# Performance work log

Measured on AMD Instinct MI355X. Metric: run time of the kernel, lower is better.

Reference implementation:

```python
import jax, jax.numpy as jnp
import numpy as np

N = 50000   # nodes
E = 800000  # edges (before self loops)
G = 8       # graphs in batch
IN, H, HD = 3, 64, 128


def setup_inputs() -> dict:
    key = jax.random.key(0)
    ks = jax.random.split(key, 12)
    s = 0.1  # weight scale
    return {
        "x": jax.random.normal(ks[0], (N, IN), jnp.float32),
        "edge_index": jax.random.randint(ks[1], (2, E), 0, N, dtype=jnp.int32),
        "batch": jnp.sort(jax.random.randint(ks[2], (N,), 0, G, dtype=jnp.int32)),
        "W1": s * jax.random.normal(ks[3], (IN, H), jnp.float32),
        "a_src1": s * jax.random.normal(ks[4], (H,), jnp.float32),
        "a_dst1": s * jax.random.normal(ks[5], (H,), jnp.float32),
        "b1": jnp.zeros((H,), jnp.float32),
        "W2": s * jax.random.normal(ks[6], (H, H), jnp.float32),
        "a_src2": s * jax.random.normal(ks[7], (H,), jnp.float32),
        "a_dst2": s * jax.random.normal(ks[8], (H,), jnp.float32),
        "b2": jnp.zeros((H,), jnp.float32),
        "Wh1": s * jax.random.normal(ks[9], (H, HD), jnp.float32),
        "bh1": jnp.zeros((HD,), jnp.float32),
        "Wh2": s * jax.random.normal(ks[10], (HD, 1), jnp.float32),
        "bh2": jnp.zeros((1,), jnp.float32),
    }


def gat_conv(x, src, dst, W, a_src, a_dst, b, n_nodes):
    """Single-head GATConv (PyG defaults: slope 0.2, self-loops, bias)."""
    h = x @ W                           # [N, H]
    e_s = h @ a_src                     # [N] per-node source logits
    e_d = h @ a_dst                     # [N] per-node target logits
    e = jax.nn.leaky_relu(e_s[src] + e_d[dst], 0.2)  # [E']
    # segment softmax over incoming edges of each target node
    m = jax.ops.segment_max(e, dst, num_segments=n_nodes)
    ex = jnp.exp(e - m[dst])
    denom = jax.ops.segment_sum(ex, dst, num_segments=n_nodes)
    alpha = ex / denom[dst]             # [E']
    out = jax.ops.segment_sum(h[src] * alpha[:, None], dst, num_segments=n_nodes)
    return out + b


def reference(x, edge_index, batch, W1, a_src1, a_dst1, b1,
              W2, a_src2, a_dst2, b2, Wh1, bh1, Wh2, bh2):
    n = x.shape[0]
    loops = jnp.arange(n, dtype=edge_index.dtype)
    src = jnp.concatenate([edge_index[0], loops])  # add self loops
    dst = jnp.concatenate([edge_index[1], loops])

    h = jax.nn.relu(gat_conv(x, src, dst, W1, a_src1, a_dst1, b1, n))
    h = jax.nn.relu(gat_conv(h, src, dst, W2, a_src2, a_dst2, b2, n))

    # global mean pool per graph
    sums = jax.ops.segment_sum(h, batch, num_segments=G)          # [G, H]
    cnt = jax.ops.segment_sum(jnp.ones((n,), h.dtype), batch, num_segments=G)
    pooled = sums / jnp.maximum(cnt, 1.0)[:, None]

    # value head: Linear -> ReLU -> Linear
    return jax.nn.relu(pooled @ Wh1 + bh1) @ Wh2 + bh2            # [G, 1]
```

## Files before the change

kernel.cpp:

```cpp
#include <hip/hip_runtime.h>
#include <math.h>

#define NN 50000
#define NE 800000
#define NG 8
#define H 64
#define HD 128
#define CAP 48
#define NSLICE 64
#define EPT 8
#define ETH (NE / EPT)
#define ECHUNKS ((ETH + 255) / 256)
#define NODEB ((NN * H) / 256)
#define NPB 1536
#define GB 2500
#define GSTRIDE (GB * 4)
#define NBUCK 200
#define BNODES 250
#define RCAP 4800
#define LCAP 32
#define ZWORDS (NBUCK + NSLICE*NG*H + NSLICE*NG)

typedef unsigned short ushort_t;
typedef _Float16 half_t;
typedef _Float16 half2_t __attribute__((ext_vector_type(2)));
typedef int int4v __attribute__((ext_vector_type(4)));

__global__ void k_zero(unsigned* __restrict__ p) {
    int i = blockIdx.x * blockDim.x + threadIdx.x;
    for (; i < ZWORDS; i += gridDim.x * blockDim.x) p[i] = 0u;
}

__global__ void k_binA(const int* __restrict__ src, const int* __restrict__ dst,
                       unsigned* __restrict__ cursor, unsigned* __restrict__ recs) {
    __shared__ unsigned lcnt[NBUCK];
    __shared__ unsigned lbuf[NBUCK][LCAP];
    int bid = blockIdx.x;
    for (int i = threadIdx.x; i < NBUCK; i += 256) lcnt[i] = 0;
    __syncthreads();
    int t = bid * 256 + threadIdx.x;
    int e0 = t * EPT;
    if (e0 < NE) {
        int4v da = *(const int4v*)(dst + e0);
        int4v db = *(const int4v*)(dst + e0 + 4);
        int4v sa = *(const int4v*)(src + e0);
        int4v sb = *(const int4v*)(src + e0 + 4);
        int ds[8] = {da.x, da.y, da.z, da.w, db.x, db.y, db.z, db.w};
        int ss[8] = {sa.x, sa.y, sa.z, sa.w, sb.x, sb.y, sb.z, sb.w};
        #pragma unroll
        for (int i = 0; i < 8; ++i) {
            unsigned d = (unsigned)ds[i];
            unsigned bk = d / BNODES;
            unsigned dloc = d - bk * BNODES;
            unsigned rec = ((unsigned)ss[i] << 8) | dloc;
            unsigned l = atomicAdd(&lcnt[bk], 1u);
            if (l < LCAP) lbuf[bk][l] = rec;
            else {
                unsigned g = atomicAdd(&cursor[bk], 1u);
                if (g < RCAP) recs[(size_t)bk * RCAP + g] = rec;
            }
        }
    }
    __syncthreads();
    for (int b = threadIdx.x; b < NBUCK; b += 256) {
        unsigned c = lcnt[b]; c = c > LCAP ? LCAP : c;
        if (c) {
            unsigned base = atomicAdd(&cursor[b], c);
            for (unsigned i = 0; i < c; ++i)
                if (base + i < RCAP) recs[(size_t)b * RCAP + base + i] = lbuf[b][i];
        }
    }
}

__global__ void k_buildB(const unsigned* __restrict__ cursor, const unsigned* __restrict__ recs,
                         ushort_t* __restrict__ csr, int* __restrict__ deg,
                         const float* __restrict__ x, const float* __restrict__ W,
                         const float* __restrict__ asrc, const float* __restrict__ adst,
                         const float* __restrict__ W2, half2_t* __restrict__ W2p,
                         half_t* __restrict__ h, float* __restrict__ es, float* __restrict__ ed) {
    __shared__ unsigned lcnt[BNODES];
    __shared__ ushort_t lcsr[BNODES * CAP];
    int bid = blockIdx.x;
    if (bid < NBUCK) {
        int b = bid;
        for (int i = threadIdx.x; i < BNODES; i += 256) lcnt[i] = 0;
        __syncthreads();
        unsigned total = cursor[b]; if (total > RCAP) total = RCAP;
        for (unsigned i = threadIdx.x; i < total; i += 256) {
            unsigned rec = recs[(size_t)b * RCAP + i];
            unsigned dloc = rec & 255u;
            unsigned srcv = rec >> 8;
            unsigned slot = atomicAdd(&lcnt[dloc], 1u);
            if (slot < CAP) lcsr[dloc * CAP + slot] = (ushort_t)srcv;
        }
        __syncthreads();
        const unsigned* ls = (const unsigned*)lcsr;
        unsigned* gc = (unsigned*)(csr + (size_t)b * BNODES * CAP);
        for (int i = threadIdx.x; i < BNODES * CAP / 2; i += 256) gc[i] = ls[i];
        for (int d = threadIdx.x; d < BNODES; d += 256) {
            unsigned c = lcnt[d];
            deg[b * BNODES + d] = c > CAP ? CAP : (int)c;
        }
    } else if (bid < NBUCK + NPB) {
        for (int nb = bid - NBUCK; nb < NODEB; nb += NPB) {
            int nid = nb * 256 + threadIdx.x;
            int node = nid >> 6, lane = nid & 63;
            if (node < NN) {
                float x0 = x[node*3+0], x1 = x[node*3+1], x2 = x[node*3+2];
                float hv = x0*W[lane] + x1*W[64+lane] + x2*W[128+lane];
                __builtin_nontemporal_store((half_t)hv, h + (size_t)node*64 + lane);
                float s = hv * asrc[lane], d = hv * adst[lane];
                #pragma unroll
                for (int o = 32; o > 0; o >>= 1) { s += __shfl_xor(s, o); d += __shfl_xor(d, o); }
                if (lane == 0) { es[node] = s; ed[node] = d; }
            }
        }
    } else {
        for (int i = threadIdx.x; i < (H/2) * 64; i += 256) {
            int k2 = i >> 6, ln = i & 63;
            half2_t v;
            v.x = (_Float16)W2[(2*k2)*64 + ln];
            v.y = (_Float16)W2[(2*k2+1)*64 + ln];
            W2p[i] = v;
        }
    }
}

#define GPREFETCH(node_nx)                                                       \
    int nN = 0, s0N = 0; float hsN = 0.f, ednN = 0.f, esnN = 0.f, esgN = 0.f;    \
    if ((node_nx) < NN) {                                                        \
        nN   = deg[node_nx];                                                     \
        hsN  = (float)hH[(size_t)(node_nx)*64 + lane];                           \
        ednN = ed[node_nx]; esnN = es[node_nx];                                  \
        s0N  = csr[(size_t)(node_nx) * CAP + lane];                              \
        esgN = es[s0N];                                                          \
    }

#define GPROLOGUE(node0)                                                         \
    int nC = 0, s0C = 0; float hsC = 0.f, ednC = 0.f, esnC = 0.f, esgC = 0.f;    \
    if ((node0) < NN) {                                                          \
        nC   = deg[node0]; nC = nC > CAP ? CAP : nC;                             \
        hsC  = (float)hH[(size_t)(node0)*64 + lane];                             \
        ednC = ed[node0]; esnC = es[node0];                                      \
        s0C  = csr[(size_t)(node0) * CAP + lane];                                \
        esgC = es[s0C];                                                          \
    }

#define GROTATE                                                                  \
    nC = nN > CAP ? CAP : nN; s0C = s0N; hsC = hsN; ednC = ednN; esnC = esnN;    \
    esgC = esgN;

#define CHUNK1(c)                                                                \
    {                                                                            \
        int r = (c) * 4 + sub;                                                   \
        float q = (r < nC) ? sp[r] : 0.f;                                        \
        int idx = (r < nC) ? sidx[r] : 0;                                        \
        float2 raw = *(const float2*)(hH + (size_t)idx * 64 + c4);               \
        union { float2 f; half_t hh[4]; } u; u.f = raw;                          \
        acc[(c) & 3].x += (float)u.hh[0] * q;                                    \
        acc[(c) & 3].y += (float)u.hh[1] * q;                                    \
        acc[(c) & 3].z += (float)u.hh[2] * q;                                    \
        acc[(c) & 3].w += (float)u.hh[3] * q;                                    \
        dq += q;                                                                 \
    }

#define GATHER_BODY                                                              \
    float e0 = esgC + ednC;                                                      \
    e0 = e0 > 0.f ? e0 : 0.2f * e0;                                              \
    float p0 = (lane < nC) ? __expf(e0) : 0.f;                                   \
    float evs = esnC + ednC; evs = evs > 0.f ? evs : 0.2f * evs;                 \
    float ps = __expf(evs);                                                      \
    sidx[lane] = s0C; sp[lane] = p0;                                             \
    int sub = lane >> 4;                                                         \
    int c4  = (lane & 15) * 4;                                                   \
    float4 acc[4];                                                               \
    acc[0] = {0,0,0,0}; acc[1] = {0,0,0,0}; acc[2] = {0,0,0,0}; acc[3] = {0,0,0,0}; \
    float dq = 0.f;                                                              \
    CHUNK1(0) CHUNK1(1) CHUNK1(2) CHUNK1(3)                                      \
    if (nC > 16) { CHUNK1(4) CHUNK1(5) CHUNK1(6) CHUNK1(7) }                     \
    if (nC > 32) { CHUNK1(8) CHUNK1(9) CHUNK1(10) CHUNK1(11) }                   \
    float4 A;                                                                    \
    A.x = acc[0].x + acc[1].x + acc[2].x + acc[3].x;                             \
    A.y = acc[0].y + acc[1].y + acc[2].y + acc[3].y;                             \
    A.z = acc[0].z + acc[1].z + acc[2].z + acc[3].z;                             \
    A.w = acc[0].w + acc[1].w + acc[2].w + acc[3].w;                             \
    _Pragma("unroll")                                                            \
    for (int o = 16; o <= 32; o <<= 1) {                                         \
        A.x += __shfl_xor(A.x, o); A.y += __shfl_xor(A.y, o);                    \
        A.z += __shfl_xor(A.z, o); A.w += __shfl_xor(A.w, o);                    \
        dq  += __shfl_xor(dq, o);                                                \
    }                                                                            \
    float inv = 1.0f / (dq + ps);                                                \
    float chs;                                                                   \
    {                                                                            \
        int srcl = lane >> 2;                                                    \
        float v0 = __shfl(A.x, srcl);                                            \
        float v1 = __shfl(A.y, srcl);                                            \
        float v2 = __shfl(A.z, srcl);                                            \
        float v3 = __shfl(A.w, srcl);                                            \
        int j = lane & 3;                                                        \
        chs = (j == 0) ? v0 : (j == 1) ? v1 : (j == 2) ? v2 : v3;                \
    }                                                                            \
    float f = fmaxf((chs + ps * hsC) * inv + bl, 0.f);

__global__ void k_gather1(const int* __restrict__ deg, const ushort_t* __restrict__ csr,
                          const float* __restrict__ es, const float* __restrict__ ed,
                          const half_t* __restrict__ hH, const float* __restrict__ b,
                          const half2_t* __restrict__ W2p, const float* __restrict__ as2,
                          const float* __restrict__ ad2,
                          half_t* __restrict__ h2, float* __restrict__ es2,
                          float* __restrict__ ed2) {
    __shared__ int     s_idx[4][64];
    __shared__ float   s_p[4][64];
    __shared__ half2_t s_fh[4][32];
    int lane = threadIdx.x & 63, w = threadIdx.x >> 6;
    int*   sidx = s_idx[w];
    float* sp   = s_p[w];
    float bl = b[lane], as2l = as2[lane], ad2l = ad2[lane];

    int node0 = blockIdx.x * 4 + w;
    GPROLOGUE(node0)
    for (int node = node0; node < NN; node += GSTRIDE) {
        GPREFETCH(node + GSTRIDE)
        GATHER_BODY

        ((half_t*)s_fh[w])[lane] = (half_t)f;
        float hv = 0.f;
        #pragma unroll
        for (int k2 = 0; k2 < 32; ++k2) {
            half2_t w2v = W2p[k2*64 + lane];
            half2_t f2  = s_fh[w][k2];
#if __has_builtin(__builtin_amdgcn_fdot2)
            hv = __builtin_amdgcn_fdot2(f2, w2v, hv, false);
#else
            hv += (float)f2.x * (float)w2v.x + (float)f2.y * (float)w2v.y;
#endif
        }
        h2[(size_t)node*64 + lane] = (half_t)hv;
        float ss = hv * as2l, dd = hv * ad2l;
        #pragma unroll
        for (int o = 32; o > 0; o >>= 1) {
            ss += __shfl_xor(ss, o); dd += __shfl_xor(dd, o);
        }
        if (lane == 0) { es2[node] = ss; ed2[node] = dd; }
        GROTATE
    }
}

__global__ void k_gather2(const int* __restrict__ deg, const ushort_t* __restrict__ csr,
                          const float* __restrict__ es, const float* __restrict__ ed,
                          const half_t* __restrict__ hH, const float* __restrict__ b,
                          const int* __restrict__ batch,
                          float* __restrict__ sums, float* __restrict__ cnt) {
    __shared__ int   s_idx[4][64];
    __shared__ float s_p[4][64];
    __shared__ float part[NG * H];
    __shared__ float pc[NG];
    for (int i = threadIdx.x; i < NG * H; i += 256) part[i] = 0.f;
    if (threadIdx.x < NG) pc[threadIdx.x] = 0.f;
    __syncthreads();

    int lane = threadIdx.x & 63, w = threadIdx.x >> 6;
    int*   sidx = s_idx[w];
    float* sp   = s_p[w];
    float bl = b[lane];

    int node0 = blockIdx.x * 4 + w;
    GPROLOGUE(node0)
    int gC = (node0 < NN) ? batch[node0] : 0;
    for (int node = node0; node < NN; node += GSTRIDE) {
        GPREFETCH(node + GSTRIDE)
        int gN = (node + GSTRIDE < NN) ? batch[node + GSTRIDE] : 0;
        GATHER_BODY

        atomicAdd(&part[gC * H + lane], f);
        if (lane == 0) atomicAdd(&pc[gC], 1.f);
        GROTATE
        gC = gN;
    }
    __syncthreads();
    int slice = blockIdx.x & (NSLICE - 1);
    float* ssum = sums + (size_t)slice * (NG * H);
    float* scnt = cnt + (size_t)slice * NG;
    for (int i = threadIdx.x; i < NG * H; i += 256) atomicAdd(&ssum[i], part[i]);
    if (threadIdx.x < NG) atomicAdd(&scnt[threadIdx.x], pc[threadIdx.x]);
}

__global__ void k_head(const float* __restrict__ sums, const float* __restrict__ cnt,
                       const float* __restrict__ Wh1, const float* __restrict__ bh1,
                       const float* __restrict__ Wh2, const float* __restrict__ bh2,
                       float* __restrict__ out) {
    __shared__ float pooled[NG * H];
    __shared__ float hidden[NG * HD];
    __shared__ float c_s[NG];
    int t = threadIdx.x;
    if (t < NG) {
        float c = 0.f;
        for (int s = 0; s < NSLICE; ++s) c += cnt[s * NG + t];
        c_s[t] = fmaxf(c, 1.f);
    }
    __syncthreads();
    for (int i = t; i < NG * H; i += blockDim.x) {
        float v = 0.f;
        for (int s = 0; s < NSLICE; ++s) v += sums[(size_t)s * (NG * H) + i];
        pooled[i] = v / c_s[i >> 6];
    }
    __syncthreads();
    for (int i = t; i < NG * HD; i += blockDim.x) {
        int g = i / HD, hd = i % HD;
        float acc = bh1[hd];
        for (int c = 0; c < H; ++c) acc += pooled[g * H + c] * Wh1[c * HD + hd];
        hidden[i] = fmaxf(acc, 0.f);
    }
    __syncthreads();
    if (t < NG) {
        float acc = bh2[0];
        for (int hd = 0; hd < HD; ++hd) acc += hidden[t * HD + hd] * Wh2[hd];
        out[t] = acc;
    }
}

extern "C" void kernel_launch(void* const* d_in, const int* in_sizes, int n_in,
                              void* d_out, int out_size, void* d_ws, size_t ws_size,
                              hipStream_t stream) {
    const float* x    = (const float*)d_in[0];
    const int*   ei   = (const int*)d_in[1];
    const int*   batch= (const int*)d_in[2];
    const float* W1   = (const float*)d_in[3];
    const float* as1  = (const float*)d_in[4];
    const float* ad1  = (const float*)d_in[5];
    const float* b1   = (const float*)d_in[6];
    const float* W2   = (const float*)d_in[7];
    const float* as2  = (const float*)d_in[8];
    const float* ad2  = (const float*)d_in[9];
    const float* b2   = (const float*)d_in[10];
    const float* Wh1  = (const float*)d_in[11];
    const float* bh1  = (const float*)d_in[12];
    const float* Wh2  = (const float*)d_in[13];
    const float* bh2  = (const float*)d_in[14];
    const int* src = ei;
    const int* dst = ei + NE;

    float* ws   = (float*)d_ws;
    half_t* h1  = (half_t*)ws;
    half_t* h2  = (half_t*)(ws + (size_t)NN*32);
    float* es1  = ws + (size_t)NN*64;
    float* ed1  = es1 + NN;
    float* es2  = ed1 + NN;
    float* ed2  = es2 + NN;
    unsigned* cursor = (unsigned*)(ed2 + NN);
    float* sums = (float*)(cursor + NBUCK);
    float* cnt  = sums + (size_t)NSLICE*NG*H;
    int*   deg  = (int*)(cnt + NSLICE*NG);
    ushort_t* csr = (ushort_t*)(deg + NN);
    half2_t* W2p  = (half2_t*)(csr + (size_t)NN*CAP);
    unsigned* recs = (unsigned*)(W2p + (H/2)*64);

    dim3 blk(256);
    int bBlocks = NBUCK + NPB + 1;

    k_zero<<<64, blk, 0, stream>>>(cursor);
    k_binA<<<ECHUNKS, blk, 0, stream>>>(src, dst, cursor, recs);
    k_buildB<<<bBlocks, blk, 0, stream>>>(cursor, recs, csr, deg,
                                          x, W1, as1, ad1, W2, W2p, h1, es1, ed1);
    k_gather1<<<GB, blk, 0, stream>>>(deg, csr, es1, ed1, h1, b1, W2p, as2, ad2,
                                      h2, es2, ed2);
    k_gather2<<<GB, blk, 0, stream>>>(deg, csr, es2, ed2, h2, b2, batch, sums, cnt);
    k_head<<<1, 256, 0, stream>>>(sums, cnt, Wh1, bh1, Wh2, bh2, (float*)d_out);
}
```

Baseline: 124.1 us.

## Prefetch first 16 neighbor feature rows for next node via double-buffered index smem

Extends the software pipeline in both gather kernels so the first four chunks of neighbor feature rows for the next node are loaded during the current node's work. Neighbor indices go into a second shared buffer that swaps each iteration. The aim is to hide the latency of the dependent csr→hH gather. The cost is more registers and shared memory, and the prologue no longer bounds-checks node0, which is safe only because the grid size guarantees node0 < NN.

Result: faster. 120.3 us (-3.1%).

```diff
diff --git a/kernel.cpp b/kernel.cpp
--- a/kernel.cpp
+++ b/kernel.cpp
@@ -126,29 +126,51 @@
     }
 }
 
+
+#define GPROLOGUE(node0)                                                         \
+    int nC = deg[node0]; nC = nC > CAP ? CAP : nC;                               \
+    float hsC = (float)hH[(size_t)(node0)*64 + lane];                            \
+    float ednC = ed[node0], esnC = es[node0];                                    \
+    int s0C = csr[(size_t)(node0) * CAP + lane];                                 \
+    float esgC = es[s0C];                                                        \
+    sidx[lane] = s0C;                                                            \
+    float2 t0C = *(const float2*)(hH + (size_t)sidx[sub]      * 64 + c4);        \
+    float2 t1C = *(const float2*)(hH + (size_t)sidx[4 + sub]  * 64 + c4);        \
+    float2 t2C = *(const float2*)(hH + (size_t)sidx[8 + sub]  * 64 + c4);        \
+    float2 t3C = *(const float2*)(hH + (size_t)sidx[12 + sub] * 64 + c4);
+
 #define GPREFETCH(node_nx)                                                       \
     int nN = 0, s0N = 0; float hsN = 0.f, ednN = 0.f, esnN = 0.f, esgN = 0.f;    \
+    float2 t0N = {0,0}, t1N = {0,0}, t2N = {0,0}, t3N = {0,0};                   \
     if ((node_nx) < NN) {                                                        \
         nN   = deg[node_nx];                                                     \
         hsN  = (float)hH[(size_t)(node_nx)*64 + lane];                           \
         ednN = ed[node_nx]; esnN = es[node_nx];                                  \
         s0N  = csr[(size_t)(node_nx) * CAP + lane];                              \
         esgN = es[s0N];                                                          \
-    }
-
-#define GPROLOGUE(node0)                                                         \
-    int nC = 0, s0C = 0; float hsC = 0.f, ednC = 0.f, esnC = 0.f, esgC = 0.f;    \
-    if ((node0) < NN) {                                                          \
-        nC   = deg[node0]; nC = nC > CAP ? CAP : nC;                             \
-        hsC  = (float)hH[(size_t)(node0)*64 + lane];                             \
-        ednC = ed[node0]; esnC = es[node0];                                      \
-        s0C  = csr[(size_t)(node0) * CAP + lane];                                \
-        esgC = es[s0C];                                                          \
+        sidxN[lane] = s0N;                                                       \
+        t0N = *(const float2*)(hH + (size_t)sidxN[sub]      * 64 + c4);          \
+        t1N = *(const float2*)(hH + (size_t)sidxN[4 + sub]  * 64 + c4);          \
+        t2N = *(const float2*)(hH + (size_t)sidxN[8 + sub]  * 64 + c4);          \
+        t3N = *(const float2*)(hH + (size_t)sidxN[12 + sub] * 64 + c4);          \
     }
 
 #define GROTATE                                                                  \
     nC = nN > CAP ? CAP : nN; s0C = s0N; hsC = hsN; ednC = ednN; esnC = esnN;    \
-    esgC = esgN;
+    esgC = esgN; t0C = t0N; t1C = t1N; t2C = t2N; t3C = t3N;                     \
+    { int* tmp_ = sidx; sidx = sidxN; sidxN = tmp_; }
+
+#define CHUNKP(c, tv)                                                            \
+    {                                                                            \
+        int r = (c) * 4 + sub;                                                   \
+        float q = (r < nC) ? sp[r] : 0.f;                                        \
+        union { float2 f; half_t hh[4]; } u; u.f = (tv);                         \
+        acc[(c) & 3].x += (float)u.hh[0] * q;                                    \
+        acc[(c) & 3].y += (float)u.hh[1] * q;                                    \
+        acc[(c) & 3].z += (float)u.hh[2] * q;                                    \
+        acc[(c) & 3].w += (float)u.hh[3] * q;                                    \
+        dq += q;                                                                 \
+    }
 
 #define CHUNK1(c)                                                                \
     {                                                                            \
@@ -170,13 +192,11 @@
     float p0 = (lane < nC) ? __expf(e0) : 0.f;                                   \
     float evs = esnC + ednC; evs = evs > 0.f ? evs : 0.2f * evs;                 \
     float ps = __expf(evs);                                                      \
-    sidx[lane] = s0C; sp[lane] = p0;                                             \
-    int sub = lane >> 4;                                                         \
-    int c4  = (lane & 15) * 4;                                                   \
+    sp[lane] = p0;                                                               \
     float4 acc[4];                                                               \
     acc[0] = {0,0,0,0}; acc[1] = {0,0,0,0}; acc[2] = {0,0,0,0}; acc[3] = {0,0,0,0}; \
     float dq = 0.f;                                                              \
-    CHUNK1(0) CHUNK1(1) CHUNK1(2) CHUNK1(3)                                      \
+    CHUNKP(0, t0C) CHUNKP(1, t1C) CHUNKP(2, t2C) CHUNKP(3, t3C)                  \
     if (nC > 16) { CHUNK1(4) CHUNK1(5) CHUNK1(6) CHUNK1(7) }                     \
     if (nC > 32) { CHUNK1(8) CHUNK1(9) CHUNK1(10) CHUNK1(11) }                   \
     float4 A;                                                                    \
@@ -210,12 +230,15 @@
                           const float* __restrict__ ad2,
                           half_t* __restrict__ h2, float* __restrict__ es2,
                           float* __restrict__ ed2) {
-    __shared__ int     s_idx[4][64];
+    __shared__ int     s_idxA[4][64], s_idxB[4][64];
     __shared__ float   s_p[4][64];
     __shared__ half2_t s_fh[4][32];
     int lane = threadIdx.x & 63, w = threadIdx.x >> 6;
-    int*   sidx = s_idx[w];
-    float* sp   = s_p[w];
+    int* sidx  = s_idxA[w];
+    int* sidxN = s_idxB[w];
+    float* sp  = s_p[w];
+    int sub = lane >> 4;
+    int c4  = (lane & 15) * 4;
     float bl = b[lane], as2l = as2[lane], ad2l = ad2[lane];
 
     int node0 = blockIdx.x * 4 + w;
@@ -252,7 +275,7 @@
                           const half_t* __restrict__ hH, const float* __restrict__ b,
                           const int* __restrict__ batch,
                           float* __restrict__ sums, float* __restrict__ cnt) {
-    __shared__ int   s_idx[4][64];
+    __shared__ int   s_idxA[4][64], s_idxB[4][64];
     __shared__ float s_p[4][64];
     __shared__ float part[NG * H];
     __shared__ float pc[NG];
@@ -261,13 +284,16 @@
     __syncthreads();
 
     int lane = threadIdx.x & 63, w = threadIdx.x >> 6;
-    int*   sidx = s_idx[w];
-    float* sp   = s_p[w];
+    int* sidx  = s_idxA[w];
+    int* sidxN = s_idxB[w];
+    float* sp  = s_p[w];
+    int sub = lane >> 4;
+    int c4  = (lane & 15) * 4;
     float bl = b[lane];
 
     int node0 = blockIdx.x * 4 + w;
     GPROLOGUE(node0)
-    int gC = (node0 < NN) ? batch[node0] : 0;
+    int gC = batch[node0];
     for (int node = node0; node < NN; node += GSTRIDE) {
         GPREFETCH(node + GSTRIDE)
         int gN = (node + GSTRIDE < NN) ? batch[node + GSTRIDE] : 0;
```
